# Kernel optimization log

Hardware: AMD Instinct MI355X
Metric: run time of the kernel (lower is better)

## Reference

```python
import jax, jax.numpy as jnp
import numpy as np

D = 1024
H = 16
HD = D // H
DFF = 4 * D
LN_EPS = 1e-5

def layernorm(x, gamma, beta):
    mu = jnp.mean(x, axis=-1, keepdims=True)
    var = jnp.mean(jnp.square(x - mu), axis=-1, keepdims=True)
    return (x - mu) * jax.lax.rsqrt(var + LN_EPS) * gamma + beta

def setup_inputs() -> dict:
    key = jax.random.key(0)
    ks = jax.random.split(key, 10)
    B, Nq, Nk = 2, 2048, 2048
    s = 0.02
    return {
        "q_x": jax.random.normal(ks[0], (B, Nq, D), jnp.float32),
        "kv_x": jax.random.normal(ks[1], (B, Nk, D), jnp.float32),
        "Wq": jax.random.normal(ks[2], (D, D), jnp.float32) * s,
        "Wkv": jax.random.normal(ks[3], (2 * D, D), jnp.float32) * s,
        "Wo": jax.random.normal(ks[4], (D, D), jnp.float32) * s,
        "bo": jnp.zeros((D,), jnp.float32),
        "ln_q_g": jnp.ones((D,), jnp.float32),
        "ln_q_b": jnp.zeros((D,), jnp.float32),
        "ln_kv_g": jnp.ones((D,), jnp.float32),
        "ln_kv_b": jnp.zeros((D,), jnp.float32),
        "W1": jax.random.normal(ks[5], (DFF, D), jnp.float32) * s,
        "b1": jnp.zeros((DFF,), jnp.float32),
        "W2": jax.random.normal(ks[6], (D, DFF), jnp.float32) * s,
        "b2": jnp.zeros((D,), jnp.float32),
    }

def reference(q_x, kv_x, Wq, Wkv, Wo, bo, ln_q_g, ln_q_b, ln_kv_g, ln_kv_b, W1, b1, W2, b2):
    B, Nq, _ = q_x.shape
    Nk = kv_x.shape[1]
    scale = HD ** -0.5
    # norm + projections
    q = layernorm(q_x, ln_q_g, ln_q_b) @ Wq.T                    # [B,Nq,D]
    kv = layernorm(kv_x, ln_kv_g, ln_kv_b) @ Wkv.T               # [B,Nk,2D]
    q = q.reshape(B, Nq, H, HD).transpose(0, 2, 1, 3)            # [B,H,Nq,hd]
    kv = kv.reshape(B, Nk, 2, H, HD).transpose(2, 0, 3, 1, 4)    # [2,B,H,Nk,hd]
    k, v = kv[0], kv[1]
    attn = jnp.einsum('bhqd,bhkd->bhqk', q, k) * scale           # [B,H,Nq,Nk]
    attn = jax.nn.softmax(attn, axis=-1)
    out = jnp.einsum('bhqk,bhkd->bhqd', attn, v)
    out = out.transpose(0, 2, 1, 3).reshape(B, Nq, D)
    x = q_x + out @ Wo.T + bo
    h = jax.nn.silu(x @ W1.T + b1)
    x = x + h @ W2.T + b2
    return x
```

## Files before the change

### kernel.cpp

```cpp
#include <hip/hip_runtime.h>

using u16   = unsigned short;
using f32x4 = __attribute__((ext_vector_type(4))) float;
using s16x8 = __attribute__((ext_vector_type(8))) short;
using u32x2 = __attribute__((ext_vector_type(2))) unsigned int;
using u32x4 = __attribute__((ext_vector_type(4))) unsigned int;

#define LOG2E 1.44269504088896f

static __device__ __forceinline__ u16 f2bf(float f) {
  union { float f; unsigned u; } a; a.f = f;
  unsigned r = a.u + 0x7fffu + ((a.u >> 16) & 1u);
  return (u16)(r >> 16);
}
static __device__ __forceinline__ unsigned cvtpk(float lo, float hi) {
  unsigned r;
  asm("v_cvt_pk_bf16_f32 %0, %1, %2" : "=v"(r) : "v"(lo), "v"(hi));
  return r;
}

static __device__ __forceinline__ void gload16(const void* g, void* l) {
  __builtin_amdgcn_global_load_lds(
      (__attribute__((address_space(1))) unsigned int*)g,
      (__attribute__((address_space(3))) unsigned int*)l, 16, 0, 0);
}

static __device__ __forceinline__ int xcd_swz(int b, int nb) {
  return (b & 7) * (nb >> 3) + (b >> 3);
}

__global__ __launch_bounds__(256) void prep_k(
    const float* __restrict__ Wq, const float* __restrict__ Wkv,
    const float* __restrict__ Wo, const float* __restrict__ W1,
    const float* __restrict__ W2,
    u16* __restrict__ wq_b, u16* __restrict__ wkv_b, u16* __restrict__ wo_b,
    u16* __restrict__ w1_b, u16* __restrict__ w2_b,
    const float* __restrict__ xq, const float* __restrict__ xk,
    const float* __restrict__ gq, const float* __restrict__ bq,
    const float* __restrict__ gk, const float* __restrict__ bk,
    u16* __restrict__ oq, u16* __restrict__ ok)
{
  const int blk = blockIdx.x, t = threadIdx.x;
  if (blk < 12288) {
    const int i = blk * 256 + t;
    const float* src; u16* dst; int off; float sc = 1.0f;
    if      (i <  262144) { src = Wq;  dst = wq_b;  off = i; sc = 0.125f * LOG2E; }
    else if (i <  786432) { src = Wkv; dst = wkv_b; off = i -  262144; }
    else if (i < 1048576) { src = Wo;  dst = wo_b;  off = i -  786432; }
    else if (i < 2097152) { src = W1;  dst = w1_b;  off = i - 1048576; }
    else                  { src = W2;  dst = w2_b;  off = i - 2097152; }
    const float4 v = ((const float4*)src)[off];
    ushort4 o;
    o.x = f2bf(v.x * sc); o.y = f2bf(v.y * sc); o.z = f2bf(v.z * sc); o.w = f2bf(v.w * sc);
    ((ushort4*)dst)[off] = o;
    return;
  }
  int row = blk - 12288;
  const float* x; const float* gam; const float* bet; u16* out;
  if (row < 4096) { x = xq; gam = gq; bet = bq; out = oq; }
  else { row -= 4096; x = xk; gam = gk; bet = bk; out = ok; }
  const float4 v = ((const float4*)(x + (size_t)row * 1024))[t];
  float s  = v.x + v.y + v.z + v.w;
  float ss = v.x*v.x + v.y*v.y + v.z*v.z + v.w*v.w;
  #pragma unroll
  for (int m = 1; m < 64; m <<= 1) { s += __shfl_xor(s, m); ss += __shfl_xor(ss, m); }
  __shared__ float red[8];
  const int w = t >> 6;
  if ((t & 63) == 0) { red[w] = s; red[4 + w] = ss; }
  __syncthreads();
  s  = red[0] + red[1] + red[2] + red[3];
  ss = red[4] + red[5] + red[6] + red[7];
  const float mu   = s * (1.0f / 1024.0f);
  const float rstd = rsqrtf(ss * (1.0f / 1024.0f) - mu * mu + 1e-5f);
  const float4 gv = ((const float4*)gam)[t];
  const float4 bv = ((const float4*)bet)[t];
  ushort4 o;
  o.x = f2bf((v.x - mu) * rstd * gv.x + bv.x);
  o.y = f2bf((v.y - mu) * rstd * gv.y + bv.y);
  o.z = f2bf((v.z - mu) * rstd * gv.z + bv.z);
  o.w = f2bf((v.w - mu) * rstd * gv.w + bv.w);
  ((ushort4*)(out + (size_t)row * 1024))[t] = o;
}

template<int BIAS, int RES, int SILU, int OF32, int OBF>
static __device__ __forceinline__ void gemm_body64_2buf(
    const u16* __restrict__ A, const u16* __restrict__ B,
    u16* __restrict__ Cb, float* __restrict__ Cf,
    const float* __restrict__ bias, const float* __restrict__ resid,
    int N, int K, int bid, u16* smem)
{
  const int tid = threadIdx.x;
  const int w = tid >> 6, l = tid & 63;
  const int g = l >> 4, q = l & 15;
  const int ntn = N >> 6;
  const int bm = bid / ntn, bn = bid - bm * ntn;
  const int wr = w >> 1, wc = w & 1;
  const int sw = (q & 7) << 4;
  f32x4 acc[2][2] = {};

  const size_t abase = (size_t)(bm * 128) * K;
  const size_t bbase = (size_t)(bn * 64) * K;

  auto stage = [&](int buf, int k0) {
    u16* as = smem + buf * 8192;
    u16* bs = smem + 16384 + buf * 4096;
    #pragma unroll
    for (int r = 0; r < 2; ++r) {
      const int c = (r << 9) + tid;
      const int row = c >> 3;
      const int sp = (c & 7) ^ (row & 7);
      gload16(A + abase + (size_t)row * K + k0 + sp * 8,
              as + (size_t)((r << 9) + (w << 6)) * 8);
    }
    const int row = tid >> 3;
    const int sp = (tid & 7) ^ (row & 7);
    gload16(B + bbase + (size_t)row * K + k0 + sp * 8,
            bs + (size_t)(w << 6) * 8);
  };

  const int NT = K >> 6;
  stage(0, 0);
  asm volatile("s_waitcnt vmcnt(0)" ::: "memory");
  __syncthreads();
  int cur = 0;
  for (int t = 0; t < NT; ++t) {
    if (t + 1 < NT) stage(cur ^ 1, (t + 1) << 6);
    const char* as = (const char*)(smem + cur * 8192);
    const char* bs = (const char*)(smem + 16384 + cur * 4096);
    #pragma unroll
    for (int ks = 0; ks < 2; ++ks) {
      s16x8 af[2], bfr[2];
      #pragma unroll
      for (int m = 0; m < 2; ++m)
        af[m] = *(const s16x8*)(as + (size_t)(wr * 32 + m * 16 + q) * 128 +
                                ((ks * 64 + g * 16) ^ sw));
      #pragma unroll
      for (int n = 0; n < 2; ++n)
        bfr[n] = *(const s16x8*)(bs + (size_t)(wc * 32 + n * 16 + q) * 128 +
                                 ((ks * 64 + g * 16) ^ sw));
      #pragma unroll
      for (int m = 0; m < 2; ++m)
        #pragma unroll
        for (int n = 0; n < 2; ++n)
          acc[m][n] = __builtin_amdgcn_mfma_f32_16x16x32_bf16(af[m], bfr[n], acc[m][n], 0, 0, 0);
    }
    asm volatile("s_waitcnt vmcnt(0)" ::: "memory");
    __syncthreads();
    cur ^= 1;
  }

  #pragma unroll
  for (int m = 0; m < 2; ++m) {
    const int row0 = bm * 128 + wr * 32 + m * 16 + g * 4;
    #pragma unroll
    for (int n = 0; n < 2; ++n) {
      const int col = bn * 64 + wc * 32 + n * 16 + q;
      float bv = 0.0f;
      if (BIAS) bv = bias[col];
      #pragma unroll
      for (int r = 0; r < 4; ++r) {
        const size_t idx = (size_t)(row0 + r) * N + col;
        float v = acc[m][n][r] + bv;
        if (RES)  v += resid[idx];
        if (SILU) v = v / (1.0f + __expf(-v));
        if (OF32) Cf[idx] = v;
        if (OBF)  Cb[idx] = f2bf(v);
      }
    }
  }
}

template<int BIAS, int RES, int SILU, int OF32, int OBF>
__global__ __launch_bounds__(512, 4) void gemm_k2(
    const u16* __restrict__ A, const u16* __restrict__ B,
    u16* __restrict__ Cb, float* __restrict__ Cf,
    const float* __restrict__ bias, const float* __restrict__ resid,
    int N, int K)
{
  __shared__ u16 smem[24576];
  const int bid = xcd_swz(blockIdx.x, gridDim.x);
  gemm_body64_2buf<BIAS, RES, SILU, OF32, OBF>(A, B, Cb, Cf, bias, resid, N, K, bid, smem);
}

__global__ __launch_bounds__(512, 4) void gemm_qkv_k(
    const u16* __restrict__ lnq, const u16* __restrict__ wq, u16* __restrict__ qp,
    const u16* __restrict__ lnk, const u16* __restrict__ wkv, u16* __restrict__ kvp)
{
  __shared__ u16 smem[24576];
  const int sbid = xcd_swz(blockIdx.x, 1536);
  if (sbid < 512)
    gemm_body64_2buf<0,0,0,0,1>(lnq, wq, qp, nullptr, nullptr, nullptr, 1024, 1024,
                                sbid, smem);
  else
    gemm_body64_2buf<0,0,0,0,1>(lnk, wkv, kvp, nullptr, nullptr, nullptr, 2048, 1024,
                                sbid - 512, smem);
}

template<int BIAS, int RES, int SILU, int OF32, int OBF>
__global__ __launch_bounds__(512, 4) void gemm_k3(
    const u16* __restrict__ A, const u16* __restrict__ B,
    u16* __restrict__ Cb, float* __restrict__ Cf,
    const float* __restrict__ bias, const float* __restrict__ resid,
    int N, int K)
{
  __shared__ u16 smem[36864];
  const int bid = xcd_swz(blockIdx.x, gridDim.x);
  const int tid = threadIdx.x;
  const int w = tid >> 6, l = tid & 63;
  const int g = l >> 4, q = l & 15;
  const int ntn = N >> 6;
  const int bm = bid / ntn, bn = bid - bm * ntn;
  const int wr = w >> 1, wc = w & 1;
  const int sw = (q & 7) << 4;
  f32x4 acc[2][2] = {};

  const size_t abase = (size_t)(bm * 128) * K;
  const size_t bbase = (size_t)(bn * 64) * K;

  auto stage = [&](int buf, int k0) {
    u16* as = smem + buf * 8192;
    u16* bs = smem + 24576 + buf * 4096;
    #pragma unroll
    for (int r = 0; r < 2; ++r) {
      const int c = (r << 9) + tid;
      const int row = c >> 3;
      const int sp = (c & 7) ^ (row & 7);
      gload16(A + abase + (size_t)row * K + k0 + sp * 8,
              as + (size_t)((r << 9) + (w << 6)) * 8);
    }
    const int row = tid >> 3;
    const int sp = (tid & 7) ^ (row & 7);
    gload16(B + bbase + (size_t)row * K + k0 + sp * 8,
            bs + (size_t)(w << 6) * 8);
  };

  const int NT = K >> 6;
  stage(0, 0);
  stage(1, 64);
  int cur = 0;
  for (int t = 0; t < NT; ++t) {
    if (t + 1 < NT) asm volatile("s_waitcnt vmcnt(3)" ::: "memory");
    else            asm volatile("s_waitcnt vmcnt(0)" ::: "memory");
    __builtin_amdgcn_s_barrier();
    asm volatile("" ::: "memory");
    if (t + 2 < NT) stage((cur == 0) ? 2 : cur - 1, (t + 2) << 6);

    const char* as = (const char*)(smem + cur * 8192);
    const char* bs = (const char*)(smem + 24576 + cur * 4096);
    #pragma unroll
    for (int ks = 0; ks < 2; ++ks) {
      s16x8 af[2], bfr[2];
      #pragma unroll
      for (int m = 0; m < 2; ++m)
        af[m] = *(const s16x8*)(as + (size_t)(wr * 32 + m * 16 + q) * 128 +
                                ((ks * 64 + g * 16) ^ sw));
      #pragma unroll
      for (int n = 0; n < 2; ++n)
        bfr[n] = *(const s16x8*)(bs + (size_t)(wc * 32 + n * 16 + q) * 128 +
                                 ((ks * 64 + g * 16) ^ sw));
      __builtin_amdgcn_s_setprio(1);
      #pragma unroll
      for (int m = 0; m < 2; ++m)
        #pragma unroll
        for (int n = 0; n < 2; ++n)
          acc[m][n] = __builtin_amdgcn_mfma_f32_16x16x32_bf16(af[m], bfr[n], acc[m][n], 0, 0, 0);
      __builtin_amdgcn_s_setprio(0);
    }
    cur = (cur == 2) ? 0 : cur + 1;
  }

  #pragma unroll
  for (int m = 0; m < 2; ++m) {
    const int row0 = bm * 128 + wr * 32 + m * 16 + g * 4;
    #pragma unroll
    for (int n = 0; n < 2; ++n) {
      const int col = bn * 64 + wc * 32 + n * 16 + q;
      float bv = 0.0f;
      if (BIAS) bv = bias[col];
      #pragma unroll
      for (int r = 0; r < 4; ++r) {
        const size_t idx = (size_t)(row0 + r) * N + col;
        float v = acc[m][n][r] + bv;
        if (RES)  v += resid[idx];
        if (SILU) v = v / (1.0f + __expf(-v));
        if (OF32) Cf[idx] = v;
        if (OBF)  Cb[idx] = f2bf(v);
      }
    }
  }
}

template<int BIAS, int RES, int SILU, int OF32, int OBF>
__global__ __launch_bounds__(512, 2) void gemm256_k(
    const u16* __restrict__ A, const u16* __restrict__ B,
    u16* __restrict__ Cb, float* __restrict__ Cf,
    const float* __restrict__ bias, const float* __restrict__ resid,
    int N, int K)
{
  __shared__ u16 smem[65536];
  char* smem_c = (char*)smem;
  const int tid = threadIdx.x;
  const int w = tid >> 6, l = tid & 63;
  const int g = l >> 4, q = l & 15;
  const int wm = w >> 2, wn = w & 3;
  const int ntn = N >> 8;
  const int bid = xcd_swz(blockIdx.x, gridDim.x);
  const int bm = bid / ntn, bn = bid - bm * ntn;

  const size_t abase = (size_t)(bm * 256) * K;
  const size_t bbase = (size_t)(bn * 256) * K;

  f32x4 acc[8][4] = {};

  auto stage2 = [&](int buf, int kt, int part) {
    const int isB = part & 1, khalf = part >> 1;
    #pragma unroll
    for (int sub = 0; sub < 2; ++sub) {
      const int row  = sub * 128 + (tid >> 2);
      const int slot = (tid & 3) ^ ((row >> 1) & 3);
      const u16* src = (isB ? B + bbase : A + abase)
                     + (size_t)row * K + kt * 64 + khalf * 32 + slot * 8;
      char* dst = smem_c + buf * 65536 + isB * 32768 + khalf * 16384
                + sub * 8192 + w * 1024;
      gload16(src, dst);
    }
  };

  const int NT = K >> 6;
  stage2(0, 0, 0); stage2(0, 0, 1); stage2(0, 0, 2); stage2(0, 0, 3);
  int cur = 0;
  const int so = (g ^ ((q >> 1) & 3)) * 16;
  for (int t = 0; t < NT; ++t) {
    const bool pre = (t + 1 < NT);
    const char* base = smem_c + cur * 65536;
    #pragma unroll
    for (int ks = 0; ks < 2; ++ks) {
      if (ks == 0 || pre) asm volatile("s_waitcnt vmcnt(4)" ::: "memory");
      else                asm volatile("s_waitcnt vmcnt(0)" ::: "memory");
      asm volatile("" ::: "memory");
      __builtin_amdgcn_s_barrier();
      asm volatile("" ::: "memory");
      const char* Ab = base + ks * 16384;
      const char* Bb = base + 32768 + ks * 16384;
      s16x8 af[8], bf0[2];
      #pragma unroll
      for (int m = 0; m < 8; ++m)
        af[m] = *(const s16x8*)(Ab + (wm * 128 + m * 16 + q) * 64 + so);
      #pragma unroll
      for (int n = 0; n < 2; ++n)
        bf0[n] = *(const s16x8*)(Bb + (wn * 64 + n * 16 + q) * 64 + so);
      if (pre) stage2(cur ^ 1, t + 1, ks * 2);
      asm volatile("s_waitcnt lgkmcnt(0)" ::: "memory");
      __builtin_amdgcn_sched_barrier(0);
      __builtin_amdgcn_s_setprio(1);
      #pragma unroll
      for (int m = 0; m < 8; ++m) {
        acc[m][0] = __builtin_amdgcn_mfma_f32_16x16x32_bf16(af[m], bf0[0], acc[m][0], 0, 0, 0);
        acc[m][1] = __builtin_amdgcn_mfma_f32_16x16x32_bf16(af[m], bf0[1], acc[m][1], 0, 0, 0);
      }
      __builtin_amdgcn_s_setprio(0);
      s16x8 bf1[2];
      #pragma unroll
      for (int n = 0; n < 2; ++n)
        bf1[n] = *(const s16x8*)(Bb + (wn * 64 + (2 + n) * 16 + q) * 64 + so);
      if (pre) stage2(cur ^ 1, t + 1, ks * 2 + 1);
      asm volatile("s_waitcnt lgkmcnt(0)" ::: "memory");
      __builtin_amdgcn_sched_barrier(0);
      __builtin_amdgcn_s_setprio(1);
      #pragma unroll
      for (int m = 0; m < 8; ++m) {
        acc[m][2] = __builtin_amdgcn_mfma_f32_16x16x32_bf16(af[m], bf1[0], acc[m][2], 0, 0, 0);
        acc[m][3] = __builtin_amdgcn_mfma_f32_16x16x32_bf16(af[m], bf1[1], acc[m][3], 0, 0, 0);
      }
      __builtin_amdgcn_s_setprio(0);
    }
    cur ^= 1;
  }

  #pragma unroll
  for (int m = 0; m < 8; ++m) {
    const int row0 = bm * 256 + wm * 128 + m * 16 + g * 4;
    #pragma unroll
    for (int n = 0; n < 4; ++n) {
      const int col = bn * 256 + wn * 64 + n * 16 + q;
      float bv = 0.0f;
      if (BIAS) bv = bias[col];
      #pragma unroll
      for (int r = 0; r < 4; ++r) {
        const size_t idx = (size_t)(row0 + r) * N + col;
        float v = acc[m][n][r] + bv;
        if (RES)  v += resid[idx];
        if (SILU) v = v / (1.0f + __expf(-v));
        if (OF32) Cf[idx] = v;
        if (OBF)  Cb[idx] = f2bf(v);
      }
    }
  }
}

__global__ __launch_bounds__(512, 4) void attn_k(
    const u16* __restrict__ Q, const u16* __restrict__ KV, u16* __restrict__ O)
{
  __shared__ u16 Ks[3][64 * 64];
  __shared__ u16 Vs[3][64 * 64];
  const int tid = threadIdx.x;
  const int w = tid >> 6, l = tid & 63;
  const int g = l >> 4, q = l & 15;
  const int idx = blockIdx.x >> 3;
  const int bh = (blockIdx.x & 7) * 4 + (idx >> 4);
  const int qt = idx & 15;
  const int b = bh >> 4, h = bh & 15;

  const size_t qrow = (size_t)(b * 2048 + qt * 128 + w * 16 + q);
  s16x8 qf[2];
  qf[0] = *(const s16x8*)&Q[qrow * 1024 + h * 64 + g * 8];
  qf[1] = *(const s16x8*)&Q[qrow * 1024 + h * 64 + 32 + g * 8];

  f32x4 oacc[4] = {};
  f32x4 ls = {0.0f, 0.0f, 0.0f, 0.0f};

  const u16* kvb = KV + (size_t)b * 2048 * 2048;
  const unsigned vs_base =
      (unsigned)(unsigned long long)(__attribute__((address_space(3))) u16*)Vs;

  auto stage = [&](int buf, int kv0) {
    const int c = tid;
    const int krow = c >> 3, slot = c & 7;
    gload16(kvb + (size_t)(kv0 + krow) * 2048 + h * 64 + ((slot ^ (krow & 7)) << 3),
            &Ks[buf][(size_t)(w << 6) * 8]);
    const int vkv = ((c >> 3) & 15) * 4 + ((c >> 1) & 3);
    const int vd0 = ((c >> 7) & 3) * 16 + (c & 1) * 8;
    gload16(kvb + (size_t)(kv0 + vkv) * 2048 + 1024 + h * 64 + vd0,
            &Vs[buf][(size_t)(w << 6) * 8]);
  };

  stage(0, 0);
  stage(1, 64);
  int cur = 0;

  for (int kt = 0; kt < 32; ++kt) {
    if (kt < 31) asm volatile("s_waitcnt vmcnt(2)" ::: "memory");
    else         asm volatile("s_waitcnt vmcnt(0)" ::: "memory");
    __builtin_amdgcn_s_barrier();
    asm volatile("" ::: "memory");
    if (kt + 2 < 32) stage((cur == 0) ? 2 : cur - 1, (kt + 2) * 64);

    const char* ksb = (const char*)Ks[cur];
    f32x4 sacc[4] = {};
    __builtin_amdgcn_s_setprio(1);
    #pragma unroll
    for (int s = 0; s < 2; ++s)
      #pragma unroll
      for (int nf = 0; nf < 4; ++nf) {
        const int krw = nf * 16 + q;
        const s16x8 kf = *(const s16x8*)(ksb + krw * 128 +
                              ((s * 64 + g * 16) ^ ((krw & 7) << 4)));
        sacc[nf] = __builtin_amdgcn_mfma_f32_16x16x32_bf16(kf, qf[s], sacc[nf], 0, 0, 0);
      }
    __builtin_amdgcn_s_setprio(0);

    #pragma unroll
    for (int nf = 0; nf < 4; ++nf)
      #pragma unroll
      for (int r = 0; r < 4; ++r)
        sacc[nf][r] = __builtin_amdgcn_exp2f(sacc[nf][r]);
    ls += sacc[0]; ls += sacc[1]; ls += sacc[2]; ls += sacc[3];

    union { u32x4 u; s16x8 s8; } au[2];
    #pragma unroll
    for (int s = 0; s < 2; ++s) {
      au[s].u[0] = cvtpk(sacc[2*s  ][0], sacc[2*s  ][1]);
      au[s].u[1] = cvtpk(sacc[2*s  ][2], sacc[2*s  ][3]);
      au[s].u[2] = cvtpk(sacc[2*s+1][0], sacc[2*s+1][1]);
      au[s].u[3] = cvtpk(sacc[2*s+1][2], sacc[2*s+1][3]);
    }

    const unsigned a0 = vs_base + (unsigned)(cur * 8192) + (unsigned)(g * 128 + 2 * q);
    u32x2 v0,v1,v2,v3,v4,v5,v6,v7,v8,v9,v10,v11,v12,v13,v14,v15;
    asm volatile(
        "ds_read_b64_tr_b16 %0,  %16\n\t"
        "ds_read_b64_tr_b16 %1,  %16 offset:512\n\t"
        "ds_read_b64_tr_b16 %2,  %16 offset:2048\n\t"
        "ds_read_b64_tr_b16 %3,  %16 offset:2560\n\t"
        "ds_read_b64_tr_b16 %4,  %16 offset:4096\n\t"
        "ds_read_b64_tr_b16 %5,  %16 offset:4608\n\t"
        "ds_read_b64_tr_b16 %6,  %16 offset:6144\n\t"
        "ds_read_b64_tr_b16 %7,  %16 offset:6656\n\t"
        "ds_read_b64_tr_b16 %8,  %16 offset:1024\n\t"
        "ds_read_b64_tr_b16 %9,  %16 offset:1536\n\t"
        "ds_read_b64_tr_b16 %10, %16 offset:3072\n\t"
        "ds_read_b64_tr_b16 %11, %16 offset:3584\n\t"
        "ds_read_b64_tr_b16 %12, %16 offset:5120\n\t"
        "ds_read_b64_tr_b16 %13, %16 offset:5632\n\t"
        "ds_read_b64_tr_b16 %14, %16 offset:7168\n\t"
        "ds_read_b64_tr_b16 %15, %16 offset:7680\n\t"
        "s_waitcnt lgkmcnt(0)"
        : "=&v"(v0), "=&v"(v1), "=&v"(v2),  "=&v"(v3),
          "=&v"(v4), "=&v"(v5), "=&v"(v6),  "=&v"(v7),
          "=&v"(v8), "=&v"(v9), "=&v"(v10), "=&v"(v11),
          "=&v"(v12),"=&v"(v13),"=&v"(v14), "=&v"(v15)
        : "v"(a0) : "memory");
    __builtin_amdgcn_sched_barrier(0);

    __builtin_amdgcn_s_setprio(1);
    {
      union { u32x4 u; s16x8 s8; } bu;
      bu.u[0]=v0[0];  bu.u[1]=v0[1];  bu.u[2]=v1[0];  bu.u[3]=v1[1];
      oacc[0] = __builtin_amdgcn_mfma_f32_16x16x32_bf16(au[0].s8, bu.s8, oacc[0], 0, 0, 0);
      bu.u[0]=v2[0];  bu.u[1]=v2[1];  bu.u[2]=v3[0];  bu.u[3]=v3[1];
      oacc[1] = __builtin_amdgcn_mfma_f32_16x16x32_bf16(au[0].s8, bu.s8, oacc[1], 0, 0, 0);
      bu.u[0]=v4[0];  bu.u[1]=v4[1];  bu.u[2]=v5[0];  bu.u[3]=v5[1];
      oacc[2] = __builtin_amdgcn_mfma_f32_16x16x32_bf16(au[0].s8, bu.s8, oacc[2], 0, 0, 0);
      bu.u[0]=v6[0];  bu.u[1]=v6[1];  bu.u[2]=v7[0];  bu.u[3]=v7[1];
      oacc[3] = __builtin_amdgcn_mfma_f32_16x16x32_bf16(au[0].s8, bu.s8, oacc[3], 0, 0, 0);
      bu.u[0]=v8[0];  bu.u[1]=v8[1];  bu.u[2]=v9[0];  bu.u[3]=v9[1];
      oacc[0] = __builtin_amdgcn_mfma_f32_16x16x32_bf16(au[1].s8, bu.s8, oacc[0], 0, 0, 0);
      bu.u[0]=v10[0]; bu.u[1]=v10[1]; bu.u[2]=v11[0]; bu.u[3]=v11[1];
      oacc[1] = __builtin_amdgcn_mfma_f32_16x16x32_bf16(au[1].s8, bu.s8, oacc[1], 0, 0, 0);
      bu.u[0]=v12[0]; bu.u[1]=v12[1]; bu.u[2]=v13[0]; bu.u[3]=v13[1];
      oacc[2] = __builtin_amdgcn_mfma_f32_16x16x32_bf16(au[1].s8, bu.s8, oacc[2], 0, 0, 0);
      bu.u[0]=v14[0]; bu.u[1]=v14[1]; bu.u[2]=v15[0]; bu.u[3]=v15[1];
      oacc[3] = __builtin_amdgcn_mfma_f32_16x16x32_bf16(au[1].s8, bu.s8, oacc[3], 0, 0, 0);
    }
    __builtin_amdgcn_s_setprio(0);

    cur = (cur == 2) ? 0 : cur + 1;
  }

  float lsum = (ls[0] + ls[1]) + (ls[2] + ls[3]);
  lsum += __shfl_xor(lsum, 16);
  lsum += __shfl_xor(lsum, 32);
  float lr[4];
  #pragma unroll
  for (int r = 0; r < 4; ++r) lr[r] = __shfl(lsum, g * 4 + r);
  const size_t ob = (size_t)(b * 2048 + qt * 128 + w * 16) * 1024 + h * 64;
  #pragma unroll
  for (int r = 0; r < 4; ++r) {
    const float inv = 1.0f / lr[r];
    #pragma unroll
    for (int nf = 0; nf < 4; ++nf)
      O[ob + (size_t)(g * 4 + r) * 1024 + nf * 16 + q] = f2bf(oacc[nf][r] * inv);
  }
}

extern "C" void kernel_launch(void* const* d_in, const int* in_sizes, int n_in,
                              void* d_out, int out_size, void* d_ws, size_t ws_size,
                              hipStream_t stream)
{
  const float* q_x  = (const float*)d_in[0];
  const float* kv_x = (const float*)d_in[1];
  const float* Wq   = (const float*)d_in[2];
  const float* Wkv  = (const float*)d_in[3];
  const float* Wo   = (const float*)d_in[4];
  const float* bo   = (const float*)d_in[5];
  const float* lnqg = (const float*)d_in[6];
  const float* lnqb = (const float*)d_in[7];
  const float* lnkg = (const float*)d_in[8];
  const float* lnkb = (const float*)d_in[9];
  const float* W1   = (const float*)d_in[10];
  const float* b1   = (const float*)d_in[11];
  const float* W2   = (const float*)d_in[12];
  const float* b2   = (const float*)d_in[13];
  float* out = (float*)d_out;

  char* ws = (char*)d_ws;
  const size_t MB = 1024 * 1024;
  u16*   wq_b  = (u16*)  (ws +  0 * MB);
  u16*   wkv_b = (u16*)  (ws +  2 * MB);
  u16*   wo_b  = (u16*)  (ws +  6 * MB);
  u16*   w1_b  = (u16*)  (ws +  8 * MB);
  u16*   w2_b  = (u16*)  (ws + 16 * MB);
  u16*   lnq   = (u16*)  (ws + 24 * MB);
  u16*   lnk   = (u16*)  (ws + 32 * MB);
  u16*   qp    = (u16*)  (ws + 40 * MB);
  u16*   kvp   = (u16*)  (ws + 48 * MB);
  u16*   ao    = (u16*)  (ws + 64 * MB);
  float* xf    = (float*)(ws + 72 * MB);
  u16*   xb    = (u16*)  (ws + 88 * MB);
  u16*   hb    = (u16*)  (ws + 96 * MB);

  prep_k<<<dim3(20480), dim3(256), 0, stream>>>(
      Wq, Wkv, Wo, W1, W2, wq_b, wkv_b, wo_b, w1_b, w2_b,
      q_x, kv_x, lnqg, lnqb, lnkg, lnkb, lnq, lnk);

  gemm_qkv_k<<<dim3(1536), dim3(512), 0, stream>>>(lnq, wq_b, qp, lnk, wkv_b, kvp);
  attn_k<<<dim3(512), dim3(512), 0, stream>>>(qp, kvp, ao);
  gemm_k2<1,1,0,1,1><<<dim3(512),  dim3(512), 0, stream>>>(
      ao, wo_b, xb, xf, bo, q_x, 1024, 1024);
  gemm256_k<1,0,1,0,1><<<dim3(256), dim3(512), 0, stream>>>(
      xb, w1_b, hb, nullptr, b1, nullptr, 4096, 1024);
  gemm_k3<1,1,0,1,0><<<dim3(512),  dim3(512), 0, stream>>>(
      hb, w2_b, nullptr, out, b2, xf, 1024, 4096);
}
```

Baseline: 194.2 us.

## Process two query sub-tiles per warp in attention to reuse K/V tiles

Each warp in the attention kernel now handles 32 query rows (two 16-row sub-tiles) instead of 16, so each block covers 256 queries and the grid is halved to 256 blocks. Every K fragment read from LDS and every transposed V read feeds two MFMAs, halving LDS and global K/V traffic per unit of work. In exchange each thread holds twice the accumulators, so launch bounds drop to 2 blocks per CU. Only 256 blocks are launched, which may underfill the device and hurt latency hiding.

```diff
diff --git a/kernel.cpp b/kernel.cpp
--- a/kernel.cpp
+++ b/kernel.cpp
@@ -398,7 +398,7 @@
   }
 }
 
-__global__ __launch_bounds__(512, 4) void attn_k(
+__global__ __launch_bounds__(512, 2) void attn_k(
     const u16* __restrict__ Q, const u16* __restrict__ KV, u16* __restrict__ O)
 {
   __shared__ u16 Ks[3][64 * 64];
@@ -407,17 +407,21 @@
   const int w = tid >> 6, l = tid & 63;
   const int g = l >> 4, q = l & 15;
   const int idx = blockIdx.x >> 3;
-  const int bh = (blockIdx.x & 7) * 4 + (idx >> 4);
-  const int qt = idx & 15;
+  const int bh = (blockIdx.x & 7) * 4 + (idx >> 3);
+  const int qt = idx & 7;
   const int b = bh >> 4, h = bh & 15;
 
-  const size_t qrow = (size_t)(b * 2048 + qt * 128 + w * 16 + q);
-  s16x8 qf[2];
-  qf[0] = *(const s16x8*)&Q[qrow * 1024 + h * 64 + g * 8];
-  qf[1] = *(const s16x8*)&Q[qrow * 1024 + h * 64 + 32 + g * 8];
-
-  f32x4 oacc[4] = {};
-  f32x4 ls = {0.0f, 0.0f, 0.0f, 0.0f};
+  s16x8 qf[2][2];
+  #pragma unroll
+  for (int j = 0; j < 2; ++j) {
+    const size_t qrow = (size_t)(b * 2048 + qt * 256 + w * 32 + j * 16 + q);
+    qf[j][0] = *(const s16x8*)&Q[qrow * 1024 + h * 64 + g * 8];
+    qf[j][1] = *(const s16x8*)&Q[qrow * 1024 + h * 64 + 32 + g * 8];
+  }
+
+  f32x4 oacc[2][4] = {};
+  f32x4 ls0 = {0.0f, 0.0f, 0.0f, 0.0f};
+  f32x4 ls1 = {0.0f, 0.0f, 0.0f, 0.0f};
 
   const u16* kvb = KV + (size_t)b * 2048 * 2048;
   const unsigned vs_base =
@@ -446,7 +450,7 @@
     if (kt + 2 < 32) stage((cur == 0) ? 2 : cur - 1, (kt + 2) * 64);
 
     const char* ksb = (const char*)Ks[cur];
-    f32x4 sacc[4] = {};
+    f32x4 sacc[2][4] = {};
     __builtin_amdgcn_s_setprio(1);
     #pragma unroll
     for (int s = 0; s < 2; ++s)
@@ -455,25 +459,31 @@
         const int krw = nf * 16 + q;
         const s16x8 kf = *(const s16x8*)(ksb + krw * 128 +
                               ((s * 64 + g * 16) ^ ((krw & 7) << 4)));
-        sacc[nf] = __builtin_amdgcn_mfma_f32_16x16x32_bf16(kf, qf[s], sacc[nf], 0, 0, 0);
+        sacc[0][nf] = __builtin_amdgcn_mfma_f32_16x16x32_bf16(kf, qf[0][s], sacc[0][nf], 0, 0, 0);
+        sacc[1][nf] = __builtin_amdgcn_mfma_f32_16x16x32_bf16(kf, qf[1][s], sacc[1][nf], 0, 0, 0);
       }
     __builtin_amdgcn_s_setprio(0);
 
     #pragma unroll
-    for (int nf = 0; nf < 4; ++nf)
-      #pragma unroll
-      for (int r = 0; r < 4; ++r)
-        sacc[nf][r] = __builtin_amdgcn_exp2f(sacc[nf][r]);
-    ls += sacc[0]; ls += sacc[1]; ls += sacc[2]; ls += sacc[3];
-
-    union { u32x4 u; s16x8 s8; } au[2];
-    #pragma unroll
-    for (int s = 0; s < 2; ++s) {
-      au[s].u[0] = cvtpk(sacc[2*s  ][0], sacc[2*s  ][1]);
-      au[s].u[1] = cvtpk(sacc[2*s  ][2], sacc[2*s  ][3]);
-      au[s].u[2] = cvtpk(sacc[2*s+1][0], sacc[2*s+1][1]);
-      au[s].u[3] = cvtpk(sacc[2*s+1][2], sacc[2*s+1][3]);
-    }
+    for (int j = 0; j < 2; ++j)
+      #pragma unroll
+      for (int nf = 0; nf < 4; ++nf)
+        #pragma unroll
+        for (int r = 0; r < 4; ++r)
+          sacc[j][nf][r] = __builtin_amdgcn_exp2f(sacc[j][nf][r]);
+    ls0 += sacc[0][0]; ls0 += sacc[0][1]; ls0 += sacc[0][2]; ls0 += sacc[0][3];
+    ls1 += sacc[1][0]; ls1 += sacc[1][1]; ls1 += sacc[1][2]; ls1 += sacc[1][3];
+
+    union { u32x4 u; s16x8 s8; } au[2][2];
+    #pragma unroll
+    for (int j = 0; j < 2; ++j)
+      #pragma unroll
+      for (int s = 0; s < 2; ++s) {
+        au[j][s].u[0] = cvtpk(sacc[j][2*s  ][0], sacc[j][2*s  ][1]);
+        au[j][s].u[1] = cvtpk(sacc[j][2*s  ][2], sacc[j][2*s  ][3]);
+        au[j][s].u[2] = cvtpk(sacc[j][2*s+1][0], sacc[j][2*s+1][1]);
+        au[j][s].u[3] = cvtpk(sacc[j][2*s+1][2], sacc[j][2*s+1][3]);
+      }
 
     const unsigned a0 = vs_base + (unsigned)(cur * 8192) + (unsigned)(g * 128 + 2 * q);
     u32x2 v0,v1,v2,v3,v4,v5,v6,v7,v8,v9,v10,v11,v12,v13,v14,v15;
@@ -505,41 +515,48 @@
     __builtin_amdgcn_s_setprio(1);
     {
       union { u32x4 u; s16x8 s8; } bu;
-      bu.u[0]=v0[0];  bu.u[1]=v0[1];  bu.u[2]=v1[0];  bu.u[3]=v1[1];
-      oacc[0] = __builtin_amdgcn_mfma_f32_16x16x32_bf16(au[0].s8, bu.s8, oacc[0], 0, 0, 0);
-      bu.u[0]=v2[0];  bu.u[1]=v2[1];  bu.u[2]=v3[0];  bu.u[3]=v3[1];
-      oacc[1] = __builtin_amdgcn_mfma_f32_16x16x32_bf16(au[0].s8, bu.s8, oacc[1], 0, 0, 0);
-      bu.u[0]=v4[0];  bu.u[1]=v4[1];  bu.u[2]=v5[0];  bu.u[3]=v5[1];
-      oacc[2] = __builtin_amdgcn_mfma_f32_16x16x32_bf16(au[0].s8, bu.s8, oacc[2], 0, 0, 0);
-      bu.u[0]=v6[0];  bu.u[1]=v6[1];  bu.u[2]=v7[0];  bu.u[3]=v7[1];
-      oacc[3] = __builtin_amdgcn_mfma_f32_16x16x32_bf16(au[0].s8, bu.s8, oacc[3], 0, 0, 0);
-      bu.u[0]=v8[0];  bu.u[1]=v8[1];  bu.u[2]=v9[0];  bu.u[3]=v9[1];
-      oacc[0] = __builtin_amdgcn_mfma_f32_16x16x32_bf16(au[1].s8, bu.s8, oacc[0], 0, 0, 0);
-      bu.u[0]=v10[0]; bu.u[1]=v10[1]; bu.u[2]=v11[0]; bu.u[3]=v11[1];
-      oacc[1] = __builtin_amdgcn_mfma_f32_16x16x32_bf16(au[1].s8, bu.s8, oacc[1], 0, 0, 0);
-      bu.u[0]=v12[0]; bu.u[1]=v12[1]; bu.u[2]=v13[0]; bu.u[3]=v13[1];
-      oacc[2] = __builtin_amdgcn_mfma_f32_16x16x32_bf16(au[1].s8, bu.s8, oacc[2], 0, 0, 0);
-      bu.u[0]=v14[0]; bu.u[1]=v14[1]; bu.u[2]=v15[0]; bu.u[3]=v15[1];
-      oacc[3] = __builtin_amdgcn_mfma_f32_16x16x32_bf16(au[1].s8, bu.s8, oacc[3], 0, 0, 0);
+      #define PVMM(nf) \
+        oacc[0][nf] = __builtin_amdgcn_mfma_f32_16x16x32_bf16(au[0][S_].s8, bu.s8, oacc[0][nf], 0, 0, 0); \
+        oacc[1][nf] = __builtin_amdgcn_mfma_f32_16x16x32_bf16(au[1][S_].s8, bu.s8, oacc[1][nf], 0, 0, 0);
+      {
+        const int S_ = 0;
+        bu.u[0]=v0[0];  bu.u[1]=v0[1];  bu.u[2]=v1[0];  bu.u[3]=v1[1];  PVMM(0)
+        bu.u[0]=v2[0];  bu.u[1]=v2[1];  bu.u[2]=v3[0];  bu.u[3]=v3[1];  PVMM(1)
+        bu.u[0]=v4[0];  bu.u[1]=v4[1];  bu.u[2]=v5[0];  bu.u[3]=v5[1];  PVMM(2)
+        bu.u[0]=v6[0];  bu.u[1]=v6[1];  bu.u[2]=v7[0];  bu.u[3]=v7[1];  PVMM(3)
+      }
+      {
+        const int S_ = 1;
+        bu.u[0]=v8[0];  bu.u[1]=v8[1];  bu.u[2]=v9[0];  bu.u[3]=v9[1];  PVMM(0)
+        bu.u[0]=v10[0]; bu.u[1]=v10[1]; bu.u[2]=v11[0]; bu.u[3]=v11[1]; PVMM(1)
+        bu.u[0]=v12[0]; bu.u[1]=v12[1]; bu.u[2]=v13[0]; bu.u[3]=v13[1]; PVMM(2)
+        bu.u[0]=v14[0]; bu.u[1]=v14[1]; bu.u[2]=v15[0]; bu.u[3]=v15[1]; PVMM(3)
+      }
+      #undef PVMM
     }
     __builtin_amdgcn_s_setprio(0);
 
     cur = (cur == 2) ? 0 : cur + 1;
   }
 
-  float lsum = (ls[0] + ls[1]) + (ls[2] + ls[3]);
-  lsum += __shfl_xor(lsum, 16);
-  lsum += __shfl_xor(lsum, 32);
-  float lr[4];
+  float lsum0 = (ls0[0] + ls0[1]) + (ls0[2] + ls0[3]);
+  float lsum1 = (ls1[0] + ls1[1]) + (ls1[2] + ls1[3]);
+  lsum0 += __shfl_xor(lsum0, 16);  lsum0 += __shfl_xor(lsum0, 32);
+  lsum1 += __shfl_xor(lsum1, 16);  lsum1 += __shfl_xor(lsum1, 32);
   #pragma unroll
-  for (int r = 0; r < 4; ++r) lr[r] = __shfl(lsum, g * 4 + r);
-  const size_t ob = (size_t)(b * 2048 + qt * 128 + w * 16) * 1024 + h * 64;
-  #pragma unroll
-  for (int r = 0; r < 4; ++r) {
-    const float inv = 1.0f / lr[r];
-    #pragma unroll
-    for (int nf = 0; nf < 4; ++nf)
-      O[ob + (size_t)(g * 4 + r) * 1024 + nf * 16 + q] = f2bf(oacc[nf][r] * inv);
+  for (int j = 0; j < 2; ++j) {
+    float lr[4];
+    #pragma unroll
+    for (int r = 0; r < 4; ++r)
+      lr[r] = __shfl(j ? lsum1 : lsum0, g * 4 + r);
+    const size_t ob = (size_t)(b * 2048 + qt * 256 + w * 32 + j * 16) * 1024 + h * 64;
+    #pragma unroll
+    for (int r = 0; r < 4; ++r) {
+      const float inv = 1.0f / lr[r];
+      #pragma unroll
+      for (int nf = 0; nf < 4; ++nf)
+        O[ob + (size_t)(g * 4 + r) * 1024 + nf * 16 + q] = f2bf(oacc[j][nf][r] * inv);
+    }
   }
 }
 
@@ -584,7 +601,7 @@
       q_x, kv_x, lnqg, lnqb, lnkg, lnkb, lnq, lnk);
 
   gemm_qkv_k<<<dim3(1536), dim3(512), 0, stream>>>(lnq, wq_b, qp, lnk, wkv_b, kvp);
-  attn_k<<<dim3(512), dim3(512), 0, stream>>>(qp, kvp, ao);
+  attn_k<<<dim3(256), dim3(512), 0, stream>>>(qp, kvp, ao);
   gemm_k2<1,1,0,1,1><<<dim3(512),  dim3(512), 0, stream>>>(
       ao, wo_b, xb, xf, bo, q_x, 1024, 1024);
   gemm256_k<1,0,1,0,1><<<dim3(256), dim3(512), 0, stream>>>(
```

After: 199.7 us. 1.03x slower.
